# Optimization experiments

Hardware: AMD Instinct MI355X
Metric: run time of the kernel (lower is better)

## Reference

```python
import jax, jax.numpy as jnp
import numpy as np

# Static architecture of the decoded CNN (matches init_kwargs index_dict)
KERNEL_NO = [64, 128, 256]
KERNEL_SIZE = [9, 9, 9]
CH_IN = [3, 64, 128]
IDX_START = [0, 1792, 75648]
I_DIM = 370816  # last slice's last index + 1
D_MODEL = 512
BATCH = 128
N_LAYERS = len(KERNEL_NO)


def _build_slices():
    """Replicates DebedderNeuron.get_kernel_slices(); per-layer int32 index matrix [K_l, L_l]."""
    sl = []
    for idx in range(N_LAYERS):
        rows = []
        for kd in range(KERNEL_NO[idx]):
            s = IDX_START[idx] + kd * KERNEL_SIZE[idx] * CH_IN[idx]
            e = s + KERNEL_SIZE[idx] * CH_IN[idx]
            bias = IDX_START[idx] + KERNEL_NO[idx] * KERNEL_SIZE[idx] * CH_IN[idx] + kd
            ik = list(range(s, e)) + [bias]
            if idx < N_LAYERS - 1:
                for kn in range(KERNEL_NO[idx + 1]):
                    ns = (IDX_START[idx + 1] + kd * KERNEL_SIZE[idx + 1]
                          + kn * CH_IN[idx + 1] * KERNEL_SIZE[idx + 1])
                    ik.extend(range(ns, ns + KERNEL_SIZE[idx + 1]))
            rows.append(ik)
        sl.append(jnp.asarray(np.array(rows, dtype=np.int32)))
    return sl

IDX = _build_slices()  # lengths per row: [1180, 2881, 1153]


def setup_inputs() -> dict:
    key = jax.random.key(0)
    ks = jax.random.split(key, 7)
    dims = [int(IDX[l].shape[1]) for l in range(N_LAYERS)]
    inp = {"x": jax.random.normal(ks[0], (BATCH, sum(KERNEL_NO), D_MODEL), jnp.float32)}
    for l in range(N_LAYERS):
        inp[f"W{l}"] = jax.random.normal(ks[1 + 2 * l], (D_MODEL, dims[l]), jnp.float32) * 0.02
        inp[f"b{l}"] = jax.random.normal(ks[2 + 2 * l], (dims[l],), jnp.float32) * 0.02
    return inp


def reference(x, W0, b0, W1, b1, W2, b2):
    # One shared Linear per CNN layer (as in the torch module); batch all kernels of a
    # layer into a single GEMM, then scatter-add into the flat weight vector y.
    Ws = [W0, W1, W2]
    bs = [b0, b1, b2]
    y = jnp.zeros((x.shape[0], I_DIM), x.dtype)
    off = 0
    for l in range(N_LAYERS):
        K = KERNEL_NO[l]
        yt = jnp.einsum('bkd,di->bki', x[:, off:off + K], Ws[l]) + bs[l]  # [B, K_l, L_l]
        y = y.at[:, IDX[l]].add(yt)  # overlapping scatter-add, matches sequential += in torch
        off += K
    # middle layers are written twice (own slice + previous layer's extension) -> halve
    y = y.at[:, IDX_START[1]:IDX_START[-1]].multiply(0.5)
    return y
```

## Files before the change

### kernel.cpp

```cpp
#include <hip/hip_runtime.h>
#include <cstdint>

typedef short short8 __attribute__((ext_vector_type(8)));
typedef float f32x4 __attribute__((ext_vector_type(4)));

#define LDS_AS3(p) ((__attribute__((address_space(3))) unsigned*)(p))
#define GLB_AS1(p) ((const __attribute__((address_space(1))) unsigned*)(p))

__device__ inline unsigned bfpack(float a, float b) {
    union { float f; unsigned u; } ua, ub;
    ua.f = a; ub.f = b;
    unsigned lo = (ua.u + 0x7FFFu + ((ua.u >> 16) & 1u)) >> 16;
    unsigned hi = (ub.u + 0x7FFFu + ((ub.u >> 16) & 1u)) & 0xFFFF0000u;
    return lo | hi;
}

__global__ __launch_bounds__(256)
void cvt_x(const float* __restrict__ X, unsigned short* __restrict__ XB)
{
    const int g = blockIdx.x * 256 + threadIdx.x;
    const float4 v0 = *(const float4*)(X + (size_t)g * 8);
    const float4 v1 = *(const float4*)(X + (size_t)g * 8 + 4);
    uint4 u;
    u.x = bfpack(v0.x, v0.y); u.y = bfpack(v0.z, v0.w);
    u.z = bfpack(v1.x, v1.y); u.w = bfpack(v1.z, v1.w);
    *(uint4*)(XB + (size_t)g * 8) = u;
}

template <int N>
__global__ __launch_bounds__(256)
void cvt_w(const float* __restrict__ W, unsigned short* __restrict__ WT)
{
    const int g = blockIdx.x * 256 + threadIdx.x;
    if (g >= N * 64) return;
    const int n = g % N, d8 = g / N;
    const float* p = W + (size_t)d8 * 8 * N + n;
    uint4 u;
    u.x = bfpack(p[0],             p[(size_t)N]);
    u.y = bfpack(p[2 * (size_t)N], p[3 * (size_t)N]);
    u.z = bfpack(p[4 * (size_t)N], p[5 * (size_t)N]);
    u.w = bfpack(p[6 * (size_t)N], p[7 * (size_t)N]);
    *(uint4*)(WT + (size_t)n * 512 + d8 * 8) = u;
}

__device__ inline int swzc(int row, int kg) { return row * 4 + (kg ^ ((row >> 1) & 3)); }

template <int MODE, bool PRE>
__global__ __launch_bounds__(256)
void gemm_scatter(const float* __restrict__ X, const float* __restrict__ W,
                  const unsigned short* __restrict__ XB,
                  const unsigned short* __restrict__ WT,
                  const float* __restrict__ BIAS, float* __restrict__ Y)
{
    constexpr int K_L  = (MODE == 0) ? 64 : (MODE == 1) ? 128 : 256;
    constexpr int LOGK = (MODE == 0) ? 6  : (MODE == 1) ? 7   : 8;
    constexpr int N    = (MODE == 0) ? 1180 : (MODE == 1) ? 2881 : 1153;
    constexpr int XOFF = (MODE == 0) ? 0 : (MODE == 1) ? 64 : 192;
    constexpr int NT   = (N + 127) / 128;

    __shared__ __align__(16) unsigned short lA[128 * 32];
    __shared__ __align__(16) unsigned short lB[128 * 32];

    const int t    = threadIdx.x;
    const int lane = t & 63;
    const int wave = t >> 6;
    const int wr   = wave >> 1, wc = wave & 1;
    const int nt   = blockIdx.x % NT;
    const int mt   = blockIdx.x / NT;
    const int m0   = mt * 128;
    const int n0   = nt * 128;

    f32x4 acc[4][4] = {};

    for (int kk = 0; kk < 512; kk += 32) {
        if constexpr (PRE) {
            #pragma unroll
            for (int i = 0; i < 2; ++i) {
                const int cidx = i * 256 + t;
                const int row  = cidx >> 2;
                const int kgl  = (cidx & 3) ^ ((row >> 1) & 3);
                const int m    = m0 + row;
                const int b    = m >> LOGK;
                const int kd   = m & (K_L - 1);
                const unsigned short* gp =
                    XB + ((size_t)(b * 448 + XOFF + kd) << 9) + kk + kgl * 8;
                __builtin_amdgcn_global_load_lds(GLB_AS1(gp), LDS_AS3(lA + cidx * 8), 16, 0, 0);
            }
            #pragma unroll
            for (int i = 0; i < 2; ++i) {
                const int cidx = i * 256 + t;
                const int row  = cidx >> 2;
                const int kgl  = (cidx & 3) ^ ((row >> 1) & 3);
                int gc = n0 + row; if (gc > N - 1) gc = N - 1;
                const unsigned short* gp = WT + (size_t)gc * 512 + kk + kgl * 8;
                __builtin_amdgcn_global_load_lds(GLB_AS1(gp), LDS_AS3(lB + cidx * 8), 16, 0, 0);
            }
        } else {
            #pragma unroll
            for (int i = 0; i < 4; ++i) {
                int c = t + i * 256, row = c >> 3, k4 = (c & 7) << 2;
                int m = m0 + row, b = m >> LOGK, kd = m & (K_L - 1);
                const float4 v = *(const float4*)(X + ((size_t)(b * 448 + XOFF + kd) << 9) + kk + k4);
                uint2 u; u.x = bfpack(v.x, v.y); u.y = bfpack(v.z, v.w);
                *(uint2*)((char*)lA + swzc(row, k4 >> 3) * 16 + ((k4 & 4) << 1)) = u;
            }
            #pragma unroll
            for (int i = 0; i < 2; ++i) {
                int tau = t + i * 256, kg = tau >> 7, n = tau & 127;
                int gc = n0 + n; if (gc > N - 1) gc = N - 1;
                const float* p = W + (size_t)(kk + kg * 8) * N + gc;
                uint4 u;
                u.x = bfpack(p[0], p[(size_t)N]);
                u.y = bfpack(p[2 * (size_t)N], p[3 * (size_t)N]);
                u.z = bfpack(p[4 * (size_t)N], p[5 * (size_t)N]);
                u.w = bfpack(p[6 * (size_t)N], p[7 * (size_t)N]);
                *(uint4*)((char*)lB + swzc(n, kg) * 16) = u;
            }
        }
        __syncthreads();

        const int kgl  = lane >> 4;
        const int lr16 = lane & 15;
        short8 af[4], bfr[4];
        #pragma unroll
        for (int mi = 0; mi < 4; ++mi) {
            const int row = wr * 64 + mi * 16 + lr16;
            af[mi] = *(const short8*)(lA + swzc(row, kgl) * 8);
        }
        #pragma unroll
        for (int ni = 0; ni < 4; ++ni) {
            const int row = wc * 64 + ni * 16 + lr16;
            bfr[ni] = *(const short8*)(lB + swzc(row, kgl) * 8);
        }
        #pragma unroll
        for (int mi = 0; mi < 4; ++mi)
            #pragma unroll
            for (int ni = 0; ni < 4; ++ni)
                acc[mi][ni] = __builtin_amdgcn_mfma_f32_16x16x32_bf16(
                    af[mi], bfr[ni], acc[mi][ni], 0, 0, 0);
        __syncthreads();
    }

    const int lr = lane & 15;
    const int lq = lane >> 4;
    #pragma unroll
    for (int ni = 0; ni < 4; ++ni) {
        const int n = n0 + wc * 64 + ni * 16 + lr;
        if (n >= N) continue;
        const float bias = BIAS[n];
        #pragma unroll
        for (int mi = 0; mi < 4; ++mi) {
            #pragma unroll
            for (int r = 0; r < 4; ++r) {
                const int m  = m0 + wr * 64 + mi * 16 + lq * 4 + r;
                const int b  = m >> LOGK;
                const int kd = m & (K_L - 1);
                const float v = acc[mi][ni][r] + bias;
                float* yb = Y + (size_t)b * 370816;
                if (MODE == 0) {
                    if (n < 27)       yb[kd * 27 + n] = v;
                    else if (n == 27) yb[1728 + kd]   = v;
                    else {
                        int tt = n - 28, kn = tt / 9, j = tt - kn * 9;
                        yb[1792 + kn * 576 + kd * 9 + j] = 0.5f * v;
                    }
                } else if (MODE == 1) {
                    if (n < 576)       yb[1792 + kd * 576 + n] += 0.5f * v;
                    else if (n == 576) yb[75520 + kd] = 0.5f * v;
                    else {
                        int tt = n - 577, kn = tt / 9, j = tt - kn * 9;
                        yb[75648 + kn * 1152 + kd * 9 + j] = v;
                    }
                } else {
                    if (n < 1152) yb[75648 + kd * 1152 + n] += v;
                    else          yb[370560 + kd] = v;
                }
            }
        }
    }
}

extern "C" void kernel_launch(void* const* d_in, const int* in_sizes, int n_in,
                              void* d_out, int out_size, void* d_ws, size_t ws_size,
                              hipStream_t stream)
{
    const float* x  = (const float*)d_in[0];
    const float* W0 = (const float*)d_in[1];
    const float* b0 = (const float*)d_in[2];
    const float* W1 = (const float*)d_in[3];
    const float* b1 = (const float*)d_in[4];
    const float* W2 = (const float*)d_in[5];
    const float* b2 = (const float*)d_in[6];
    float* y = (float*)d_out;

    unsigned short* XB  = (unsigned short*)d_ws;
    unsigned short* WT0 = XB  + (size_t)128 * 448 * 512;
    unsigned short* WT1 = WT0 + (size_t)1180 * 512;
    unsigned short* WT2 = WT1 + (size_t)2881 * 512;
    const size_t NEED = ((size_t)128 * 448 * 512 + (size_t)(1180 + 2881 + 1153) * 512) * 2;

    if (ws_size >= NEED) {
        cvt_x<<<dim3(14336), 256, 0, stream>>>(x, XB);
        cvt_w<1180><<<dim3((1180 * 64 + 255) / 256), 256, 0, stream>>>(W0, WT0);
        cvt_w<2881><<<dim3((2881 * 64 + 255) / 256), 256, 0, stream>>>(W1, WT1);
        cvt_w<1153><<<dim3((1153 * 64 + 255) / 256), 256, 0, stream>>>(W2, WT2);
        gemm_scatter<0, true><<<dim3(64 * 10),  256, 0, stream>>>(x, W0, XB, WT0, b0, y);
        gemm_scatter<1, true><<<dim3(128 * 23), 256, 0, stream>>>(x, W1, XB, WT1, b1, y);
        gemm_scatter<2, true><<<dim3(256 * 10), 256, 0, stream>>>(x, W2, XB, WT2, b2, y);
    } else {
        gemm_scatter<0, false><<<dim3(64 * 10),  256, 0, stream>>>(x, W0, XB, WT0, b0, y);
        gemm_scatter<1, false><<<dim3(128 * 23), 256, 0, stream>>>(x, W1, XB, WT1, b1, y);
        gemm_scatter<2, false><<<dim3(256 * 10), 256, 0, stream>>>(x, W2, XB, WT2, b2, y);
    }
}
```

Measured before the change: 310.2 us.

## Fuse x bf16 conversion into GEMM with double-buffered LDS and XCD remap

Drops the separate x-to-bf16 conversion kernel. Each GEMM now loads fp32 x rows into registers, converts them, and writes them to LDS. The main loop is double-buffered: the next A and B tiles are loaded while MFMAs run on the current buffer, and W tiles still arrive through direct global-to-LDS loads. Block indices are remapped across 8 XCDs to improve L2 locality. The cost is that fp32 x (twice the bytes of bf16) is re-read by every N-tile, LDS use doubles, and the no-workspace fallback path is removed.

```diff
diff --git a/kernel.cpp b/kernel.cpp
--- a/kernel.cpp
+++ b/kernel.cpp
@@ -13,18 +13,6 @@
     unsigned lo = (ua.u + 0x7FFFu + ((ua.u >> 16) & 1u)) >> 16;
     unsigned hi = (ub.u + 0x7FFFu + ((ub.u >> 16) & 1u)) & 0xFFFF0000u;
     return lo | hi;
-}
-
-__global__ __launch_bounds__(256)
-void cvt_x(const float* __restrict__ X, unsigned short* __restrict__ XB)
-{
-    const int g = blockIdx.x * 256 + threadIdx.x;
-    const float4 v0 = *(const float4*)(X + (size_t)g * 8);
-    const float4 v1 = *(const float4*)(X + (size_t)g * 8 + 4);
-    uint4 u;
-    u.x = bfpack(v0.x, v0.y); u.y = bfpack(v0.z, v0.w);
-    u.z = bfpack(v1.x, v1.y); u.w = bfpack(v1.z, v1.w);
-    *(uint4*)(XB + (size_t)g * 8) = u;
 }
 
 template <int N>
@@ -43,12 +31,9 @@
     *(uint4*)(WT + (size_t)n * 512 + d8 * 8) = u;
 }
 
-__device__ inline int swzc(int row, int kg) { return row * 4 + (kg ^ ((row >> 1) & 3)); }
-
-template <int MODE, bool PRE>
+template <int MODE>
 __global__ __launch_bounds__(256)
-void gemm_scatter(const float* __restrict__ X, const float* __restrict__ W,
-                  const unsigned short* __restrict__ XB,
+void gemm_scatter(const float* __restrict__ X,
                   const unsigned short* __restrict__ WT,
                   const float* __restrict__ BIAS, float* __restrict__ Y)
 {
@@ -58,79 +43,89 @@
     constexpr int XOFF = (MODE == 0) ? 0 : (MODE == 1) ? 64 : 192;
     constexpr int NT   = (N + 127) / 128;
 
-    __shared__ __align__(16) unsigned short lA[128 * 32];
-    __shared__ __align__(16) unsigned short lB[128 * 32];
+    __shared__ __align__(16) unsigned short lA[2][128 * 32];
+    __shared__ __align__(16) unsigned short lB[2][128 * 32];
 
     const int t    = threadIdx.x;
     const int lane = t & 63;
     const int wave = t >> 6;
     const int wr   = wave >> 1, wc = wave & 1;
-    const int nt   = blockIdx.x % NT;
-    const int mt   = blockIdx.x / NT;
-    const int m0   = mt * 128;
-    const int n0   = nt * 128;
+
+    const int cpx = (int)gridDim.x >> 3;
+    const int wg  = (blockIdx.x & 7) * cpx + (blockIdx.x >> 3);
+    const int nt  = wg % NT;
+    const int mt  = wg / NT;
+    const int m0  = mt * 128;
+    const int n0  = nt * 128;
 
     f32x4 acc[4][4] = {};
-
-    for (int kk = 0; kk < 512; kk += 32) {
-        if constexpr (PRE) {
-            #pragma unroll
-            for (int i = 0; i < 2; ++i) {
-                const int cidx = i * 256 + t;
-                const int row  = cidx >> 2;
-                const int kgl  = (cidx & 3) ^ ((row >> 1) & 3);
-                const int m    = m0 + row;
-                const int b    = m >> LOGK;
-                const int kd   = m & (K_L - 1);
-                const unsigned short* gp =
-                    XB + ((size_t)(b * 448 + XOFF + kd) << 9) + kk + kgl * 8;
-                __builtin_amdgcn_global_load_lds(GLB_AS1(gp), LDS_AS3(lA + cidx * 8), 16, 0, 0);
-            }
-            #pragma unroll
-            for (int i = 0; i < 2; ++i) {
-                const int cidx = i * 256 + t;
-                const int row  = cidx >> 2;
-                const int kgl  = (cidx & 3) ^ ((row >> 1) & 3);
-                int gc = n0 + row; if (gc > N - 1) gc = N - 1;
-                const unsigned short* gp = WT + (size_t)gc * 512 + kk + kgl * 8;
-                __builtin_amdgcn_global_load_lds(GLB_AS1(gp), LDS_AS3(lB + cidx * 8), 16, 0, 0);
-            }
-        } else {
-            #pragma unroll
-            for (int i = 0; i < 4; ++i) {
-                int c = t + i * 256, row = c >> 3, k4 = (c & 7) << 2;
-                int m = m0 + row, b = m >> LOGK, kd = m & (K_L - 1);
-                const float4 v = *(const float4*)(X + ((size_t)(b * 448 + XOFF + kd) << 9) + kk + k4);
-                uint2 u; u.x = bfpack(v.x, v.y); u.y = bfpack(v.z, v.w);
-                *(uint2*)((char*)lA + swzc(row, k4 >> 3) * 16 + ((k4 & 4) << 1)) = u;
-            }
-            #pragma unroll
-            for (int i = 0; i < 2; ++i) {
-                int tau = t + i * 256, kg = tau >> 7, n = tau & 127;
-                int gc = n0 + n; if (gc > N - 1) gc = N - 1;
-                const float* p = W + (size_t)(kk + kg * 8) * N + gc;
-                uint4 u;
-                u.x = bfpack(p[0], p[(size_t)N]);
-                u.y = bfpack(p[2 * (size_t)N], p[3 * (size_t)N]);
-                u.z = bfpack(p[4 * (size_t)N], p[5 * (size_t)N]);
-                u.w = bfpack(p[6 * (size_t)N], p[7 * (size_t)N]);
-                *(uint4*)((char*)lB + swzc(n, kg) * 16) = u;
-            }
-        }
-        __syncthreads();
-
+    float4 av[2][2];
+
+    auto loadA = [&](int kk) {
+        #pragma unroll
+        for (int i = 0; i < 2; ++i) {
+            const int cidx = i * 256 + t;
+            const int row  = cidx >> 2;
+            const int kg   = cidx & 3;
+            const int m    = m0 + row;
+            const int b    = m >> LOGK;
+            const int kd   = m & (K_L - 1);
+            const float* p = X + ((size_t)(b * 448 + XOFF + kd) << 9) + kk + kg * 8;
+            av[i][0] = *(const float4*)p;
+            av[i][1] = *(const float4*)(p + 4);
+        }
+    };
+    auto writeA = [&](int buf) {
+        #pragma unroll
+        for (int i = 0; i < 2; ++i) {
+            const int cidx = i * 256 + t;
+            const int row  = cidx >> 2;
+            const int slot = (cidx & 3) ^ ((row >> 1) & 3);
+            uint4 u;
+            u.x = bfpack(av[i][0].x, av[i][0].y);
+            u.y = bfpack(av[i][0].z, av[i][0].w);
+            u.z = bfpack(av[i][1].x, av[i][1].y);
+            u.w = bfpack(av[i][1].z, av[i][1].w);
+            *(uint4*)(&lA[buf][(row * 4 + slot) * 8]) = u;
+        }
+    };
+    auto stageB = [&](int buf, int kk) {
+        #pragma unroll
+        for (int i = 0; i < 2; ++i) {
+            const int cidx = i * 256 + t;
+            const int row  = cidx >> 2;
+            const int kgl  = (cidx & 3) ^ ((row >> 1) & 3);
+            int gc = n0 + row; if (gc > N - 1) gc = N - 1;
+            const unsigned short* gp = WT + (size_t)gc * 512 + kk + kgl * 8;
+            __builtin_amdgcn_global_load_lds(GLB_AS1(gp), LDS_AS3(&lB[buf][cidx * 8]), 16, 0, 0);
+        }
+    };
+
+    loadA(0);
+    stageB(0, 0);
+    writeA(0);
+    __syncthreads();
+
+    int cur = 0;
+    #pragma unroll 1
+    for (int ks = 0; ks < 16; ++ks) {
+        const int nxt = cur ^ 1;
+        if (ks < 15) {
+            loadA((ks + 1) * 32);
+            stageB(nxt, (ks + 1) * 32);
+        }
         const int kgl  = lane >> 4;
         const int lr16 = lane & 15;
         short8 af[4], bfr[4];
         #pragma unroll
         for (int mi = 0; mi < 4; ++mi) {
             const int row = wr * 64 + mi * 16 + lr16;
-            af[mi] = *(const short8*)(lA + swzc(row, kgl) * 8);
+            af[mi] = *(const short8*)(&lA[cur][(row * 4 + (kgl ^ ((row >> 1) & 3))) * 8]);
         }
         #pragma unroll
         for (int ni = 0; ni < 4; ++ni) {
             const int row = wc * 64 + ni * 16 + lr16;
-            bfr[ni] = *(const short8*)(lB + swzc(row, kgl) * 8);
+            bfr[ni] = *(const short8*)(&lB[cur][(row * 4 + (kgl ^ ((row >> 1) & 3))) * 8]);
         }
         #pragma unroll
         for (int mi = 0; mi < 4; ++mi)
@@ -138,7 +133,11 @@
             for (int ni = 0; ni < 4; ++ni)
                 acc[mi][ni] = __builtin_amdgcn_mfma_f32_16x16x32_bf16(
                     af[mi], bfr[ni], acc[mi][ni], 0, 0, 0);
-        __syncthreads();
+        if (ks < 15) {
+            writeA(nxt);
+            __syncthreads();
+        }
+        cur = nxt;
     }
 
     const int lr = lane & 15;
@@ -193,23 +192,17 @@
     const float* b2 = (const float*)d_in[6];
     float* y = (float*)d_out;
 
-    unsigned short* XB  = (unsigned short*)d_ws;
-    unsigned short* WT0 = XB  + (size_t)128 * 448 * 512;
+    unsigned short* WT0 = (unsigned short*)d_ws;
     unsigned short* WT1 = WT0 + (size_t)1180 * 512;
     unsigned short* WT2 = WT1 + (size_t)2881 * 512;
-    const size_t NEED = ((size_t)128 * 448 * 512 + (size_t)(1180 + 2881 + 1153) * 512) * 2;
-
-    if (ws_size >= NEED) {
-        cvt_x<<<dim3(14336), 256, 0, stream>>>(x, XB);
-        cvt_w<1180><<<dim3((1180 * 64 + 255) / 256), 256, 0, stream>>>(W0, WT0);
-        cvt_w<2881><<<dim3((2881 * 64 + 255) / 256), 256, 0, stream>>>(W1, WT1);
-        cvt_w<1153><<<dim3((1153 * 64 + 255) / 256), 256, 0, stream>>>(W2, WT2);
-        gemm_scatter<0, true><<<dim3(64 * 10),  256, 0, stream>>>(x, W0, XB, WT0, b0, y);
-        gemm_scatter<1, true><<<dim3(128 * 23), 256, 0, stream>>>(x, W1, XB, WT1, b1, y);
-        gemm_scatter<2, true><<<dim3(256 * 10), 256, 0, stream>>>(x, W2, XB, WT2, b2, y);
-    } else {
-        gemm_scatter<0, false><<<dim3(64 * 10),  256, 0, stream>>>(x, W0, XB, WT0, b0, y);
-        gemm_scatter<1, false><<<dim3(128 * 23), 256, 0, stream>>>(x, W1, XB, WT1, b1, y);
-        gemm_scatter<2, false><<<dim3(256 * 10), 256, 0, stream>>>(x, W2, XB, WT2, b2, y);
-    }
-}
+    const size_t NEED = (size_t)(1180 + 2881 + 1153) * 512 * 2;
+    if (ws_size < NEED) return;
+
+    cvt_w<1180><<<dim3((1180 * 64 + 255) / 256), 256, 0, stream>>>(W0, WT0);
+    cvt_w<2881><<<dim3((2881 * 64 + 255) / 256), 256, 0, stream>>>(W1, WT1);
+    cvt_w<1153><<<dim3((1153 * 64 + 255) / 256), 256, 0, stream>>>(W2, WT2);
+
+    gemm_scatter<0><<<dim3(64 * 10),  256, 0, stream>>>(x, WT0, b0, y);
+    gemm_scatter<1><<<dim3(128 * 23), 256, 0, stream>>>(x, WT1, b1, y);
+    gemm_scatter<2><<<dim3(256 * 10), 256, 0, stream>>>(x, WT2, b2, y);
+}
```

New measurement: 368.9 us. 18.9% more time.
